# Kernel optimization log

Measured on AMD Instinct MI355X. Metric: run time of the kernel, lower is better.

The kernel has to match this reference:

```python
import jax, jax.numpy as jnp
import numpy as np

B, S, M, D, H, F, E, K = 4, 1024, 1024, 1024, 16, 4096, 4, 2
DH = D // H
LB_COEF = 0.01
LN_EPS = 1e-5


def setup_inputs() -> dict:
    key = jax.random.key(0)
    ks = jax.random.split(key, 16)
    w = lambda k, shape: jax.random.normal(k, shape, jnp.float32) * 0.02
    return {
        "x": jax.random.normal(ks[0], (B, S, D), jnp.float32),
        "memory": jax.random.normal(ks[1], (B, M, D), jnp.float32),
        "sWq": w(ks[2], (D, D)), "sWk": w(ks[3], (D, D)),
        "sWv": w(ks[4], (D, D)), "sWo": w(ks[5], (D, D)),
        "cWq": w(ks[6], (D, D)), "cWk": w(ks[7], (D, D)),
        "cWv": w(ks[8], (D, D)), "cWo": w(ks[9], (D, D)),
        "Wg": w(ks[10], (E, D)),
        "W1": w(ks[11], (E, F, D)), "b1": jnp.zeros((E, F), jnp.float32),
        "W2": w(ks[12], (E, D, F)), "b2": jnp.zeros((E, D), jnp.float32),
        "ln1_g": jnp.ones((D,), jnp.float32), "ln1_b": jnp.zeros((D,), jnp.float32),
        "ln2_g": jnp.ones((D,), jnp.float32), "ln2_b": jnp.zeros((D,), jnp.float32),
        "ln3_g": jnp.ones((D,), jnp.float32), "ln3_b": jnp.zeros((D,), jnp.float32),
    }


def _ln(x, g, b):
    m = x.mean(-1, keepdims=True)
    v = ((x - m) ** 2).mean(-1, keepdims=True)
    return (x - m) * jax.lax.rsqrt(v + LN_EPS) * g + b


def _mha(q_in, k_in, v_in, Wq, Wk, Wv, Wo):
    # nn.Linear(bias=False): y = x @ W.T; split into heads [b, h, s, dh]
    def split(t):
        b, s, _ = t.shape
        return t.reshape(b, s, H, DH).transpose(0, 2, 1, 3)
    Q = split(q_in @ Wq.T)
    Kh = split(k_in @ Wk.T)
    V = split(v_in @ Wv.T)
    scores = jnp.einsum('bhqd,bhkd->bhqk', Q, Kh) / jnp.sqrt(jnp.float32(DH))
    attn = jax.nn.softmax(scores, axis=-1)  # dropout is identity in eval
    out = jnp.einsum('bhqk,bhkd->bhqd', attn, V)
    b, _, s, _ = out.shape
    out = out.transpose(0, 2, 1, 3).reshape(b, s, D)
    return out @ Wo.T


def _moe(h, Wg, W1, b1, W2, b2):
    gate_logits = h @ Wg.T                      # [B, S, E]
    gate_probs = jax.nn.softmax(gate_logits, -1)
    topk_logits, topk_idx = jax.lax.top_k(gate_logits, K)
    topk_w = jax.nn.softmax(topk_logits, -1)    # [B, S, K]
    # dense all-experts FFN (faithful to source): [B, S, E, F] hidden
    hid = jax.nn.gelu(jnp.einsum('bsd,efd->bsef', h, W1) + b1, approximate=False)
    eo = jnp.einsum('bsef,edf->bsed', hid, W2) + b2   # [B, S, E, D]
    sel = jnp.take_along_axis(eo, topk_idx[..., None], axis=2)  # [B, S, K, D]
    out = (sel * topk_w[..., None]).sum(axis=2)
    one_hot = jax.nn.one_hot(topk_idx, E, dtype=gate_probs.dtype)  # [B, S, K, E]
    load = one_hot.sum(axis=2).mean(axis=(0, 1))   # [E]
    imp = gate_probs.mean(axis=(0, 1))             # [E]
    aux = LB_COEF * (E * jnp.sum(load * imp))
    return out, aux


def reference(x, memory, sWq, sWk, sWv, sWo, cWq, cWk, cWv, cWo,
              Wg, W1, b1, W2, b2,
              ln1_g, ln1_b, ln2_g, ln2_b, ln3_g, ln3_b):
    h = _ln(x, ln1_g, ln1_b)
    x = x + _mha(h, h, h, sWq, sWk, sWv, sWo)
    h = _ln(x, ln2_g, ln2_b)
    x = x + _mha(h, memory, memory, cWq, cWk, cWv, cWo)
    h = _ln(x, ln3_g, ln3_b)
    ffn_out, aux = _moe(h, Wg, W1, b1, W2, b2)
    return (x + ffn_out, aux)
```

## Files before the change

kernel.cpp:

```cpp
#include <hip/hip_runtime.h>
#include <math.h>
#include <stdint.h>

typedef unsigned short u16;
typedef _Float16 f16;
typedef __attribute__((ext_vector_type(8))) _Float16 f16x8;
typedef __attribute__((ext_vector_type(8))) short s16x8;
typedef __attribute__((ext_vector_type(4))) float f32x4;
typedef __attribute__((ext_vector_type(4))) unsigned short u16x4;

#define DEV static __device__ __forceinline__

#define MFMA16(a, b, c) __builtin_amdgcn_mfma_f32_16x16x32_f16((a), (b), (c), 0, 0, 0)

DEV void split2(float v, u16& hi, u16& lo) {
  f16 h = (f16)v;
  f16 l = (f16)(v - (float)h);
  hi = __builtin_bit_cast(u16, h);
  lo = __builtin_bit_cast(u16, l);
}
DEV u16 f2h(float v) { f16 h = (f16)v; return __builtin_bit_cast(u16, h); }
DEV float h2f(u16 u) { f16 h = __builtin_bit_cast(f16, u); return (float)h; }

DEV void gload16(const void* gp, const void* lp) {
  typedef const __attribute__((address_space(1))) unsigned GU;
  typedef __attribute__((address_space(3))) unsigned LU;
  GU* g = (GU*)(uintptr_t)gp;
  LU* l = (LU*)(unsigned)(uintptr_t)lp;
  __builtin_amdgcn_global_load_lds(g, l, 16, 0, 0);
}

DEV int swzP(int q) { return ((q & 3) << 4) ^ (((q >> 2) & 3) << 5); }


enum { EPI3_SPLIT = 0, EPI3_RESID = 1 };

template <int EPI>
__global__ __launch_bounds__(512, 4)
void gemm3(const u16* __restrict__ Ah, const u16* __restrict__ Al,
           const u16* __restrict__ Bh, const u16* __restrict__ Bl,
           int N, int K, int ldC,
           u16* __restrict__ outh, u16* __restrict__ outl,
           float* __restrict__ outf, const float* __restrict__ resid)
{
  __shared__ alignas(16) u16 sAh[2][128 * 32], sAl[2][128 * 32];
  __shared__ alignas(16) u16 sBh[2][128 * 32], sBl[2][128 * 32];
  const int tid = threadIdx.x;
  const int wave = tid >> 6, lane = tid & 63;
  const int wr = wave >> 2, wc = wave & 3;
  const int li = lane & 15, g = lane >> 4;
  const long row0 = (long)blockIdx.y * 128;
  const int col0 = blockIdx.x * 128;

  const int srow = tid >> 2;
  const int scol = ((tid & 3) ^ ((tid >> 3) & 3)) * 8;
  const long arow = (row0 + srow) * (long)K + scol;
  const long brow = ((long)col0 + srow) * (long)K + scol;
  const u16 *gAh = Ah + arow, *gAl = Al + arow;
  const u16 *gBh = Bh + brow, *gBl = Bl + brow;
  const int wbase = wave * 512;

  const f32x4 fz = {0.f, 0.f, 0.f, 0.f};
  f32x4 acc[4][2];
#pragma unroll
  for (int m = 0; m < 4; m++)
#pragma unroll
    for (int n = 0; n < 2; n++) acc[m][n] = fz;

  const int aoff = (wr * 64 + li) * 32 + (g ^ ((li >> 1) & 3)) * 8;
  const int boff = (wc * 32 + li) * 32 + (g ^ ((li >> 1) & 3)) * 8;

  gload16(gAh, &sAh[0][wbase]);
  gload16(gAl, &sAl[0][wbase]);
  gload16(gBh, &sBh[0][wbase]);
  gload16(gBl, &sBl[0][wbase]);

  int cur = 0;
  for (int k0 = 0; k0 < K; k0 += 32, cur ^= 1) {
    __syncthreads();
    const int nxt = cur ^ 1;
    if (k0 + 32 < K) {
      gload16(gAh + k0 + 32, &sAh[nxt][wbase]);
      gload16(gAl + k0 + 32, &sAl[nxt][wbase]);
      gload16(gBh + k0 + 32, &sBh[nxt][wbase]);
      gload16(gBl + k0 + 32, &sBl[nxt][wbase]);
    }
    f16x8 ah[4], al4[4], bh[2], bl4[2];
#pragma unroll
    for (int m = 0; m < 4; m++) {
      ah[m] = *(const f16x8*)(&sAh[cur][aoff + m * 512]);
      al4[m] = *(const f16x8*)(&sAl[cur][aoff + m * 512]);
    }
#pragma unroll
    for (int n = 0; n < 2; n++) {
      bh[n] = *(const f16x8*)(&sBh[cur][boff + n * 512]);
      bl4[n] = *(const f16x8*)(&sBl[cur][boff + n * 512]);
    }
#pragma unroll
    for (int m = 0; m < 4; m++)
#pragma unroll
      for (int n = 0; n < 2; n++) {
        f32x4 t = acc[m][n];
        t = MFMA16(al4[m], bh[n], t);
        t = MFMA16(ah[m], bl4[n], t);
        t = MFMA16(ah[m], bh[n], t);
        acc[m][n] = t;
      }
  }

#pragma unroll
  for (int m = 0; m < 4; m++)
#pragma unroll
    for (int n = 0; n < 2; n++) {
      const int col = col0 + wc * 32 + n * 16 + li;
#pragma unroll
      for (int r = 0; r < 4; r++) {
        const long row = row0 + wr * 64 + m * 16 + g * 4 + r;
        const long idx = row * ldC + col;
        const float v = acc[m][n][r];
        if constexpr (EPI == EPI3_SPLIT) {
          u16 hi, lo; split2(v, hi, lo);
          outh[idx] = hi; outl[idx] = lo;
        } else {
          outf[idx] = resid[idx] + v;
        }
      }
    }
}

__global__ __launch_bounds__(256)
void vtrans(const u16* __restrict__ Vh, const u16* __restrict__ Vl,
            u16* __restrict__ Th, u16* __restrict__ Tl)
{
  __shared__ u16 t0[64][80];
  __shared__ u16 t1[64][80];
  const int kb = blockIdx.x, h = blockIdx.y, b = blockIdx.z;
  const int tid = threadIdx.x;
  const int r = tid >> 2;
  const int c = tid & 3;
  const long srow = ((long)b * 1024 + kb * 64 + r) * 3072 + h * 64;
  s16x8 a0 = *(const s16x8*)(Vh + srow + c * 8);
  s16x8 a1 = *(const s16x8*)(Vh + srow + c * 8 + 32);
  s16x8 b0 = *(const s16x8*)(Vl + srow + c * 8);
  s16x8 b1 = *(const s16x8*)(Vl + srow + c * 8 + 32);
#pragma unroll
  for (int j = 0; j < 8; j++) {
    t0[c * 8 + j][r]      = (u16)(short)a0[j];
    t0[c * 8 + 32 + j][r] = (u16)(short)a1[j];
    t1[c * 8 + j][r]      = (u16)(short)b0[j];
    t1[c * 8 + 32 + j][r] = (u16)(short)b1[j];
  }
  __syncthreads();
  const int dh = tid >> 2;
  const long drow = ((long)(b * 16 + h) * 64 + dh) * 1024 + kb * 64;
  s16x8 o0, o1;
#pragma unroll
  for (int j = 0; j < 8; j++) {
    o0[j] = (short)t0[dh][c * 8 + j];
    o1[j] = (short)t0[dh][c * 8 + 32 + j];
  }
  *(s16x8*)(Th + drow + c * 8) = o0;
  *(s16x8*)(Th + drow + c * 8 + 32) = o1;
#pragma unroll
  for (int j = 0; j < 8; j++) {
    o0[j] = (short)t1[dh][c * 8 + j];
    o1[j] = (short)t1[dh][c * 8 + 32 + j];
  }
  *(s16x8*)(Tl + drow + c * 8) = o0;
  *(s16x8*)(Tl + drow + c * 8 + 32) = o1;
}

__global__ __launch_bounds__(512, 4)
void attn3(const u16* __restrict__ Qh, const u16* __restrict__ Ql,
           const u16* __restrict__ Kbh, const u16* __restrict__ Kbl,
           const u16* __restrict__ Vth, const u16* __restrict__ Vtl,
           u16* __restrict__ AOh, u16* __restrict__ AOl)
{
  __shared__ alignas(16) u16 lKh[64 * 64], lKl[64 * 64];
  __shared__ alignas(16) u16 lVh[64 * 64], lVl[64 * 64];
  __shared__ alignas(16) u16 lPh[8 * 16 * 64], lPl[8 * 16 * 64];
  const int tid = threadIdx.x;
  const int wave = tid >> 6, lane = tid & 63;
  const int li = lane & 15, g = lane >> 4;
  const int qt = blockIdx.x, h = blockIdx.y, b = blockIdx.z;
  const int bh = b * 16 + h;
  const int LD = 3072;

  const long qrow0 = (long)b * 1024 + qt * 128 + wave * 16;
  f16x8 qfh[2], qfl[2];
#pragma unroll
  for (int kk = 0; kk < 2; kk++) {
    const long qoff = (qrow0 + li) * LD + h * 64 + kk * 32 + g * 8;
    qfh[kk] = *(const f16x8*)(Qh + qoff);
    qfl[kk] = *(const f16x8*)(Ql + qoff);
  }

  const f32x4 fz = {0.f, 0.f, 0.f, 0.f};
  float m_run[4], l_run[4];
  f32x4 oacc[4];
#pragma unroll
  for (int r = 0; r < 4; r++) { m_run[r] = -INFINITY; l_run[r] = 0.f; }
#pragma unroll
  for (int d = 0; d < 4; d++) oacc[d] = fz;

  char* cKh = (char*)lKh; char* cKl = (char*)lKl;
  char* cVh = (char*)lVh; char* cVl = (char*)lVl;
  char* cPh = (char*)lPh + wave * 2048;
  char* cPl = (char*)lPl + wave * 2048;

  const int kr = tid >> 3;
  const int kce = (tid & 7) * 8;
  const u16* kbase_h = Kbh + ((long)b * 1024 + kr) * LD + h * 64 + kce;
  const u16* kbase_l = Kbl + ((long)b * 1024 + kr) * LD + h * 64 + kce;
  const u16* vbase_h = Vth + ((long)bh * 64 + kr) * 1024 + kce;
  const u16* vbase_l = Vtl + ((long)bh * 64 + kr) * 1024 + kce;
  const int sdst = kr * 128 + ((kce * 2) ^ ((kr & 7) << 4));

  s16x8 rkh, rkl, rvh, rvl;
#define LOADT(t)                                                   \
  {                                                                \
    const long ko = (long)(t) * 64 * LD;                           \
    const int vo = (t) * 64;                                       \
    rkh = *(const s16x8*)(kbase_h + ko);                           \
    rkl = *(const s16x8*)(kbase_l + ko);                           \
    rvh = *(const s16x8*)(vbase_h + vo);                           \
    rvl = *(const s16x8*)(vbase_l + vo);                           \
  }

  LOADT(0);

  for (int t = 0; t < 16; ++t) {
    __syncthreads();
    *(s16x8*)(cKh + sdst) = rkh;
    *(s16x8*)(cKl + sdst) = rkl;
    *(s16x8*)(cVh + sdst) = rvh;
    *(s16x8*)(cVl + sdst) = rvl;
    if (t < 15) LOADT(t + 1);
    __syncthreads();

    f32x4 s[4];
#pragma unroll
    for (int cb = 0; cb < 4; cb++) {
      f32x4 tt = fz;
      const int key = cb * 16 + li;
#pragma unroll
      for (int kk = 0; kk < 2; kk++) {
        const int off = key * 128 + (((kk * 32 + g * 8) * 2) ^ ((key & 7) << 4));
        f16x8 fh = *(const f16x8*)(cKh + off);
        f16x8 fl = *(const f16x8*)(cKl + off);
        tt = MFMA16(qfl[kk], fh, tt);
        tt = MFMA16(qfh[kk], fl, tt);
        tt = MFMA16(qfh[kk], fh, tt);
      }
      s[cb] = tt;
    }
#pragma unroll
    for (int cb = 0; cb < 4; cb++)
#pragma unroll
      for (int r = 0; r < 4; r++) s[cb][r] *= 0.125f;

#pragma unroll
    for (int r = 0; r < 4; r++) {
      float mx = fmaxf(fmaxf(s[0][r], s[1][r]), fmaxf(s[2][r], s[3][r]));
      mx = fmaxf(mx, __shfl_xor(mx, 1));
      mx = fmaxf(mx, __shfl_xor(mx, 2));
      mx = fmaxf(mx, __shfl_xor(mx, 4));
      mx = fmaxf(mx, __shfl_xor(mx, 8));
      float mnew = fmaxf(m_run[r], mx);
      float sc = __expf(m_run[r] - mnew);
      m_run[r] = mnew;
      float ls = 0.f;
#pragma unroll
      for (int cb = 0; cb < 4; cb++) {
        float p = __expf(s[cb][r] - mnew);
        s[cb][r] = p;
        ls += p;
      }
      ls += __shfl_xor(ls, 1);
      ls += __shfl_xor(ls, 2);
      ls += __shfl_xor(ls, 4);
      ls += __shfl_xor(ls, 8);
      l_run[r] = l_run[r] * sc + ls;
#pragma unroll
      for (int d = 0; d < 4; d++) oacc[d][r] *= sc;
    }

#pragma unroll
    for (int cb = 0; cb < 4; cb++)
#pragma unroll
      for (int r = 0; r < 4; r++) {
        const int q = g * 4 + r;
        const int key = cb * 16 + li;
        const int off = q * 128 + ((key * 2) ^ swzP(q));
        u16 hi, lo; split2(s[cb][r], hi, lo);
        *(u16*)(cPh + off) = hi;
        *(u16*)(cPl + off) = lo;
      }

#pragma unroll
    for (int kk = 0; kk < 2; kk++) {
      const int kbyte = (kk * 32 + g * 8) * 2;
      const int poff = li * 128 + (kbyte ^ swzP(li));
      f16x8 pfh = *(const f16x8*)(cPh + poff);
      f16x8 pfl = *(const f16x8*)(cPl + poff);
#pragma unroll
      for (int d = 0; d < 4; d++) {
        const int dh = d * 16 + li;
        const int voff = dh * 128 + (kbyte ^ ((dh & 7) << 4));
        f16x8 vfh = *(const f16x8*)(cVh + voff);
        f16x8 vfl = *(const f16x8*)(cVl + voff);
        f32x4 tacc = oacc[d];
        tacc = MFMA16(pfl, vfh, tacc);
        tacc = MFMA16(pfh, vfl, tacc);
        tacc = MFMA16(pfh, vfh, tacc);
        oacc[d] = tacc;
      }
    }
  }
#undef LOADT

#pragma unroll
  for (int d = 0; d < 4; d++)
#pragma unroll
    for (int r = 0; r < 4; r++) {
      const long row = qrow0 + g * 4 + r;
      const int col = h * 64 + d * 16 + li;
      u16 hi, lo; split2(oacc[d][r] / l_run[r], hi, lo);
      AOh[row * 1024 + col] = hi;
      AOl[row * 1024 + col] = lo;
    }
}

template <bool GATE>
__global__ __launch_bounds__(256)
void ln_kernel(const float* __restrict__ x, const float* __restrict__ gam,
               const float* __restrict__ bet, u16* __restrict__ hh,
               u16* __restrict__ hl,
               const float* __restrict__ Wg, float* __restrict__ glog)
{
  const int row = blockIdx.x;
  const int tid = threadIdx.x;
  const int wave = tid >> 6, lane = tid & 63;
  const float* xr = x + (long)row * 1024;
  float4 v = *(const float4*)(xr + tid * 4);
  float s = v.x + v.y + v.z + v.w;
  float s2 = v.x * v.x + v.y * v.y + v.z * v.z + v.w * v.w;
#pragma unroll
  for (int m = 1; m < 64; m <<= 1) { s += __shfl_xor(s, m); s2 += __shfl_xor(s2, m); }
  __shared__ float red1[4], red2[4];
  if (lane == 0) { red1[wave] = s; red2[wave] = s2; }
  __syncthreads();
  float S = red1[0] + red1[1] + red1[2] + red1[3];
  float S2 = red2[0] + red2[1] + red2[2] + red2[3];
  float mean = S * (1.f / 1024.f);
  float var = S2 * (1.f / 1024.f) - mean * mean;
  float rstd = 1.f / sqrtf(var + 1e-5f);
  const int c = tid * 4;
  float hv[4];
  hv[0] = (v.x - mean) * rstd * gam[c + 0] + bet[c + 0];
  hv[1] = (v.y - mean) * rstd * gam[c + 1] + bet[c + 1];
  hv[2] = (v.z - mean) * rstd * gam[c + 2] + bet[c + 2];
  hv[3] = (v.w - mean) * rstd * gam[c + 3] + bet[c + 3];
  u16x4 oh, ol;
#pragma unroll
  for (int j = 0; j < 4; j++) {
    u16 hi, lo; split2(hv[j], hi, lo);
    oh[j] = hi; ol[j] = lo;
  }
  *(u16x4*)(hh + (long)row * 1024 + c) = oh;
  *(u16x4*)(hl + (long)row * 1024 + c) = ol;

  if constexpr (GATE) {
    float pe[4];
#pragma unroll
    for (int e = 0; e < 4; e++) {
      const float* wr_ = Wg + e * 1024 + c;
      pe[e] = hv[0] * wr_[0] + hv[1] * wr_[1] + hv[2] * wr_[2] + hv[3] * wr_[3];
    }
#pragma unroll
    for (int e = 0; e < 4; e++)
#pragma unroll
      for (int m = 1; m < 64; m <<= 1) pe[e] += __shfl_xor(pe[e], m);
    __shared__ float gred[4][4];
    if (lane == 0) {
#pragma unroll
      for (int e = 0; e < 4; e++) gred[wave][e] = pe[e];
    }
    __syncthreads();
    if (tid < 4)
      glog[(long)row * 4 + tid] = gred[0][tid] + gred[1][tid] + gred[2][tid] + gred[3][tid];
  }
}

__global__ __launch_bounds__(256)
void route_kernel(const float* __restrict__ glog,
                  int* __restrict__ tlist, float* __restrict__ wrow,
                  int4* __restrict__ meta, float2* __restrict__ wts,
                  int* __restrict__ scanMeta, float* __restrict__ outAux)
{
  const int tid = threadIdx.x;
  const int lane = tid & 63, wave = tid >> 6;
  __shared__ int scn[4][256];
  __shared__ int sTot[4];
  __shared__ int sBase[4];
  __shared__ float sred[4][8];

  for (int r = tid; r < 8704; r += 256) { tlist[r] = 0; wrow[r] = 0.f; }

  int myCnt[4] = {0, 0, 0, 0};
  float imp[4] = {0.f, 0.f, 0.f, 0.f}, ld[4] = {0.f, 0.f, 0.f, 0.f};
  unsigned char e1s[16], e2s[16];
  float w1s[16], w2s[16];
#pragma unroll 1
  for (int j = 0; j < 16; j++) {
    const int t = tid * 16 + j;
    float l[4];
#pragma unroll
    for (int e = 0; e < 4; e++) l[e] = glog[t * 4 + e];
    int e1 = 0; float bv = l[0];
#pragma unroll
    for (int e = 1; e < 4; e++) if (l[e] > bv) { bv = l[e]; e1 = e; }
    int e2 = -1; float bv2 = -INFINITY;
#pragma unroll
    for (int e = 0; e < 4; e++) if (e != e1 && l[e] > bv2) { bv2 = l[e]; e2 = e; }
    float wq = expf(bv2 - bv);
    float w1 = 1.f / (1.f + wq), w2 = wq / (1.f + wq);
    float ps = 0.f, pv[4];
#pragma unroll
    for (int e = 0; e < 4; e++) { pv[e] = expf(l[e] - bv); ps += pv[e]; }
    float inv = 1.f / ps;
#pragma unroll
    for (int e = 0; e < 4; e++) imp[e] += pv[e] * inv;
    ld[e1] += 1.f; ld[e2] += 1.f;
    myCnt[e1]++; myCnt[e2]++;
    e1s[j] = (unsigned char)e1; e2s[j] = (unsigned char)e2;
    w1s[j] = w1; w2s[j] = w2;
  }
#pragma unroll
  for (int e = 0; e < 4; e++) scn[e][tid] = myCnt[e];
  __syncthreads();

  if (wave < 4) {
    int carry = 0;
    for (int seg = 0; seg < 4; seg++) {
      int v = scn[wave][seg * 64 + lane];
      const int orig = v;
#pragma unroll
      for (int d = 1; d < 64; d <<= 1) { int o = __shfl_up(v, d); if (lane >= d) v += o; }
      scn[wave][seg * 64 + lane] = carry + v - orig;
      carry += __shfl(v, 63);
    }
    if (lane == 0) sTot[wave] = carry;
  }
  __syncthreads();

  if (tid == 0) {
    int base = 0;
    for (int e = 0; e < 4; e++) {
      const int c = sTot[e];
      const int cap = (c + 127) & ~127;
      sBase[e] = base;
      const int t0 = base >> 7, t1 = (base + cap) >> 7;
      for (int i = t0; i < t1; i++) scanMeta[1 + i] = e;
      base += cap;
    }
    scanMeta[0] = base >> 7;
  }
  __syncthreads();

  int off[4];
#pragma unroll
  for (int e = 0; e < 4; e++) off[e] = sBase[e] + scn[e][tid];
#pragma unroll 1
  for (int j = 0; j < 16; j++) {
    const int t = tid * 16 + j;
    const int e1 = e1s[j], e2 = e2s[j];
    const int p1 = off[e1]++;
    const int p2 = off[e2]++;
    tlist[p1] = t; wrow[p1] = w1s[j];
    tlist[p2] = t; wrow[p2] = w2s[j];
    int4 m; m.x = p1; m.y = p2; m.z = e1; m.w = e2;
    meta[t] = m;
    float2 w; w.x = w1s[j]; w.y = w2s[j];
    wts[t] = w;
  }

#pragma unroll
  for (int e = 0; e < 4; e++) {
#pragma unroll
    for (int d = 1; d < 64; d <<= 1) {
      imp[e] += __shfl_xor(imp[e], d);
      ld[e] += __shfl_xor(ld[e], d);
    }
  }
  if (lane == 0) {
#pragma unroll
    for (int e = 0; e < 4; e++) { sred[wave][e] = imp[e]; sred[wave][4 + e] = ld[e]; }
  }
  __syncthreads();
  if (tid == 0) {
    float a = 0.f;
    for (int e = 0; e < 4; e++) {
      float im = sred[0][e] + sred[1][e] + sred[2][e] + sred[3][e];
      float lo = sred[0][4 + e] + sred[1][4 + e] + sred[2][4 + e] + sred[3][4 + e];
      a += (lo * (1.f / 4096.f)) * (im * (1.f / 4096.f));
    }
    outAux[0] = 0.01f * 4.f * a;
  }
}

__global__ __launch_bounds__(256, 2)
void gemm_up(const u16* __restrict__ A, const u16* __restrict__ w1h,
             const float* __restrict__ b1, const int* __restrict__ tlist,
             const float* __restrict__ wrow, const int* __restrict__ scanMeta,
             u16* __restrict__ hid)
{
  const int L = blockIdx.x;
  const int gg = (L & 7) * 272 + (L >> 3);
  const int rt = gg >> 5, cc = gg & 31;
  if (rt >= scanMeta[0]) return;
  const int e = scanMeta[1 + rt];
  __shared__ alignas(16) u16 lA[2][128 * 32];
  __shared__ alignas(16) u16 lB[2][128 * 32];
  const int tid = threadIdx.x;
  const int wave = tid >> 6, lane = tid & 63;
  const int wr = wave >> 1, wc = wave & 1;
  const int li = lane & 15, g = lane >> 4;
  const int row0 = rt * 128;
  const int col0 = cc * 128;

  const int srow = lane >> 2;
  const int scol = ((lane & 3) ^ ((lane >> 3) & 3)) * 8;
  const int r1 = row0 + wave * 32 + srow;
  const long t1 = tlist[r1], t2 = tlist[r1 + 16];
  const u16* gA1 = A + t1 * 1024 + scol;
  const u16* gA2 = A + t2 * 1024 + scol;
  const u16* gB = w1h + (size_t)e * 4194304 +
                  ((size_t)(col0 + wave * 32 + srow)) * 1024 + scol;
  const int wbase = wave * 1024;

  const f32x4 fz = {0.f, 0.f, 0.f, 0.f};
  f32x4 acc[4][4];
#pragma unroll
  for (int m = 0; m < 4; m++)
#pragma unroll
    for (int n = 0; n < 4; n++) acc[m][n] = fz;

  const int aoff = (wr * 64 + li) * 32 + (g ^ ((li >> 1) & 3)) * 8;
  const int boff = (wc * 64 + li) * 32 + (g ^ ((li >> 1) & 3)) * 8;

  gload16(gA1, &lA[0][wbase]);
  gload16(gA2, &lA[0][wbase + 512]);
  gload16(gB, &lB[0][wbase]);
  gload16(gB + 16 * 1024, &lB[0][wbase + 512]);

  int cur = 0;
  for (int k0 = 0; k0 < 1024; k0 += 32, cur ^= 1) {
    __syncthreads();
    const int nxt = cur ^ 1;
    if (k0 + 32 < 1024) {
      gload16(gA1 + k0 + 32, &lA[nxt][wbase]);
      gload16(gA2 + k0 + 32, &lA[nxt][wbase + 512]);
      gload16(gB + k0 + 32, &lB[nxt][wbase]);
      gload16(gB + k0 + 32 + 16 * 1024, &lB[nxt][wbase + 512]);
    }
    f16x8 af[4], bfr[4];
#pragma unroll
    for (int m = 0; m < 4; m++) af[m] = *(const f16x8*)(&lA[cur][aoff + m * 512]);
#pragma unroll
    for (int n = 0; n < 4; n++) bfr[n] = *(const f16x8*)(&lB[cur][boff + n * 512]);
#pragma unroll
    for (int m = 0; m < 4; m++)
#pragma unroll
      for (int n = 0; n < 4; n++)
        acc[m][n] = MFMA16(af[m], bfr[n], acc[m][n]);
  }

#pragma unroll
  for (int m = 0; m < 4; m++)
#pragma unroll
    for (int n = 0; n < 4; n++) {
      const int col = col0 + wc * 64 + n * 16 + li;
#pragma unroll
      for (int r = 0; r < 4; r++) {
        const int row = row0 + wr * 64 + m * 16 + g * 4 + r;
        const float coef = wrow[row];
        float tv = acc[m][n][r] + b1[e * 4096 + col];
        float ge = 0.5f * tv * (1.f + erff(tv * 0.7071067811865475f));
        hid[(size_t)row * 4096 + col] = f2h(coef * ge);
      }
    }
}

__global__ __launch_bounds__(512, 4)
void gemm_down(const u16* __restrict__ hid, const u16* __restrict__ w2h,
               const int* __restrict__ scanMeta, u16* __restrict__ part)
{
  const int L = blockIdx.x;
  const int gg = (L & 7) * 68 + (L >> 3);
  const int rt = gg >> 3, cc = gg & 7;
  if (rt >= scanMeta[0]) return;
  const int e = scanMeta[1 + rt];
  __shared__ alignas(16) u16 lA[2][128 * 32];
  __shared__ alignas(16) u16 lB[2][128 * 32];
  const int tid = threadIdx.x;
  const int wave = tid >> 6, lane = tid & 63;
  const int wr = wave >> 2, wc = wave & 3;
  const int li = lane & 15, g = lane >> 4;
  const int row0 = rt * 128;
  const int col0 = cc * 128;

  const int srow = tid >> 2;
  const int scol = ((tid & 3) ^ ((tid >> 3) & 3)) * 8;
  const u16* gA = hid + ((size_t)(row0 + srow)) * 4096 + scol;
  const u16* gB = w2h + (size_t)e * 4194304 +
                  ((size_t)(col0 + srow)) * 4096 + scol;
  const int wbase = wave * 512;

  const f32x4 fz = {0.f, 0.f, 0.f, 0.f};
  f32x4 acc[4][2];
#pragma unroll
  for (int m = 0; m < 4; m++)
#pragma unroll
    for (int n = 0; n < 2; n++) acc[m][n] = fz;

  const int aoff = (wr * 64 + li) * 32 + (g ^ ((li >> 1) & 3)) * 8;
  const int boff = (wc * 32 + li) * 32 + (g ^ ((li >> 1) & 3)) * 8;

  gload16(gA, &lA[0][wbase]);
  gload16(gB, &lB[0][wbase]);

  int cur = 0;
  for (int k0 = 0; k0 < 4096; k0 += 32, cur ^= 1) {
    __syncthreads();
    const int nxt = cur ^ 1;
    if (k0 + 32 < 4096) {
      gload16(gA + k0 + 32, &lA[nxt][wbase]);
      gload16(gB + k0 + 32, &lB[nxt][wbase]);
    }
    f16x8 af[4], bfr[2];
#pragma unroll
    for (int m = 0; m < 4; m++) af[m] = *(const f16x8*)(&lA[cur][aoff + m * 512]);
#pragma unroll
    for (int n = 0; n < 2; n++) bfr[n] = *(const f16x8*)(&lB[cur][boff + n * 512]);
#pragma unroll
    for (int m = 0; m < 4; m++)
#pragma unroll
      for (int n = 0; n < 2; n++)
        acc[m][n] = MFMA16(af[m], bfr[n], acc[m][n]);
  }

#pragma unroll
  for (int m = 0; m < 4; m++)
#pragma unroll
    for (int n = 0; n < 2; n++) {
      const int col = col0 + wc * 32 + n * 16 + li;
#pragma unroll
      for (int r = 0; r < 4; r++) {
        const int row = row0 + wr * 64 + m * 16 + g * 4 + r;
        part[(size_t)row * 1024 + col] = f2h(acc[m][n][r]);
      }
    }
}

__global__ __launch_bounds__(256)
void merge_kernel(const float* __restrict__ xw, const u16* __restrict__ part,
                  const int4* __restrict__ meta, const float2* __restrict__ wts,
                  const float* __restrict__ b2, float* __restrict__ out)
{
  const long i = ((long)blockIdx.x * 256 + threadIdx.x) * 4;
  const int row = (int)(i >> 10), col = (int)(i & 1023);
  const int4 m = meta[row];
  const float2 w = wts[row];
  float4 a = *(const float4*)(xw + i);
  u16x4 p1 = *(const u16x4*)(part + (size_t)m.x * 1024 + col);
  u16x4 p2 = *(const u16x4*)(part + (size_t)m.y * 1024 + col);
  const float* b2a = b2 + m.z * 1024 + col;
  const float* b2b = b2 + m.w * 1024 + col;
  float av[4] = {a.x, a.y, a.z, a.w};
  float4 o;
  float ov[4];
#pragma unroll
  for (int j = 0; j < 4; j++)
    ov[j] = av[j] + h2f(p1[j]) + h2f(p2[j]) + w.x * b2a[j] + w.y * b2b[j];
  o.x = ov[0]; o.y = ov[1]; o.z = ov[2]; o.w = ov[3];
  *(float4*)(out + i) = o;
}

__global__ __launch_bounds__(256)
void cvt_h(const float* __restrict__ src, u16* __restrict__ dst)
{
  const long i = ((long)blockIdx.x * 256 + threadIdx.x) * 4;
  float4 v = *(const float4*)(src + i);
  u16x4 o = {f2h(v.x), f2h(v.y), f2h(v.z), f2h(v.w)};
  *(u16x4*)(dst + i) = o;
}

__global__ __launch_bounds__(256)
void cvt_split(const float* __restrict__ src, u16* __restrict__ dh, u16* __restrict__ dl)
{
  const long i = ((long)blockIdx.x * 256 + threadIdx.x) * 4;
  float4 v = *(const float4*)(src + i);
  u16x4 oh, ol;
  float vv[4] = {v.x, v.y, v.z, v.w};
#pragma unroll
  for (int j = 0; j < 4; j++) { u16 a, b; split2(vv[j], a, b); oh[j] = a; ol[j] = b; }
  *(u16x4*)(dh + i) = oh;
  *(u16x4*)(dl + i) = ol;
}

struct Ptr8 { const float* p[8]; };

__global__ __launch_bounds__(256)
void cvt8_split(Ptr8 ps, u16* __restrict__ dh, u16* __restrict__ dl)
{
  const int w = blockIdx.y;
  const long i = ((long)blockIdx.x * 256 + threadIdx.x) * 4;
  float4 v = *(const float4*)(ps.p[w] + i);
  u16x4 oh, ol;
  float vv[4] = {v.x, v.y, v.z, v.w};
#pragma unroll
  for (int j = 0; j < 4; j++) { u16 a, b; split2(vv[j], a, b); oh[j] = a; ol[j] = b; }
  *(u16x4*)(dh + (long)w * 1048576 + i) = oh;
  *(u16x4*)(dl + (long)w * 1048576 + i) = ol;
}

extern "C" void kernel_launch(void* const* d_in, const int* in_sizes, int n_in,
                              void* d_out, int out_size, void* d_ws, size_t ws_size,
                              hipStream_t stream)
{
  const float* x    = (const float*)d_in[0];
  const float* mem  = (const float*)d_in[1];
  const float* sWq  = (const float*)d_in[2];
  const float* sWk  = (const float*)d_in[3];
  const float* sWv  = (const float*)d_in[4];
  const float* sWo  = (const float*)d_in[5];
  const float* cWq  = (const float*)d_in[6];
  const float* cWk  = (const float*)d_in[7];
  const float* cWv  = (const float*)d_in[8];
  const float* cWo  = (const float*)d_in[9];
  const float* Wg   = (const float*)d_in[10];
  const float* W1   = (const float*)d_in[11];
  const float* b1   = (const float*)d_in[12];
  const float* W2   = (const float*)d_in[13];
  const float* b2   = (const float*)d_in[14];
  const float* ln1g = (const float*)d_in[15];
  const float* ln1b = (const float*)d_in[16];
  const float* ln2g = (const float*)d_in[17];
  const float* ln2b = (const float*)d_in[18];
  const float* ln3g = (const float*)d_in[19];
  const float* ln3b = (const float*)d_in[20];
  float* out = (float*)d_out;
  (void)in_sizes; (void)n_in; (void)out_size; (void)ws_size;

  char* ws = (char*)d_ws;
  size_t off = 0;
  auto alloc = [&](size_t bytes) -> void* {
    void* p = ws + off; off += (bytes + 255) & ~(size_t)255; return p;
  };
  float* xw    = (float*)alloc((size_t)4096 * 1024 * 4);
  u16*   hh    = (u16*)  alloc((size_t)4096 * 1024 * 2);
  u16*   hl    = (u16*)  alloc((size_t)4096 * 1024 * 2);
  u16*   memh  = (u16*)  alloc((size_t)4096 * 1024 * 2);
  u16*   meml  = (u16*)  alloc((size_t)4096 * 1024 * 2);
  u16*   qkvh  = (u16*)  alloc((size_t)4096 * 3072 * 2);
  u16*   qkvl  = (u16*)  alloc((size_t)4096 * 3072 * 2);
  u16*   aoh   = (u16*)  alloc((size_t)4096 * 1024 * 2);
  u16*   aol   = (u16*)  alloc((size_t)4096 * 1024 * 2);
  u16*   aWh   = (u16*)  alloc((size_t)8 * 1024 * 1024 * 2);
  u16*   aWl   = (u16*)  alloc((size_t)8 * 1024 * 1024 * 2);
  u16*   w1h   = (u16*)  alloc((size_t)4 * 4096 * 1024 * 2);
  u16*   w2h   = (u16*)  alloc((size_t)4 * 4096 * 1024 * 2);
  float* glog  = (float*)alloc((size_t)4096 * 4 * 4);
  int*   tlist = (int*)  alloc((size_t)8704 * 4);
  float* wrow  = (float*)alloc((size_t)8704 * 4);
  int4*  meta  = (int4*) alloc((size_t)4096 * 16);
  float2* wts  = (float2*)alloc((size_t)4096 * 8);
  int*   scanM = (int*)  alloc((size_t)128 * 4);
  u16*   vth = hh;
  u16*   vtl = hl;
  u16*   hid = qkvh;
  u16*   part = (u16*)hh;

  Ptr8 p8;
  p8.p[0] = sWq; p8.p[1] = sWk; p8.p[2] = sWv; p8.p[3] = sWo;
  p8.p[4] = cWq; p8.p[5] = cWk; p8.p[6] = cWv; p8.p[7] = cWo;
  cvt8_split<<<dim3(1024, 8), 256, 0, stream>>>(p8, aWh, aWl);
  cvt_h<<<16384, 256, 0, stream>>>(W1, w1h);
  cvt_h<<<16384, 256, 0, stream>>>(W2, w2h);
  cvt_split<<<4096, 256, 0, stream>>>(mem, memh, meml);

  ln_kernel<false><<<4096, 256, 0, stream>>>(x, ln1g, ln1b, hh, hl, nullptr, nullptr);
  gemm3<EPI3_SPLIT><<<dim3(24, 32), 512, 0, stream>>>(hh, hl, aWh, aWl, 3072, 1024, 3072,
                                                      qkvh, qkvl, nullptr, nullptr);
  vtrans<<<dim3(16, 16, 4), 256, 0, stream>>>(qkvh + 2048, qkvl + 2048, vth, vtl);
  attn3<<<dim3(8, 16, 4), 512, 0, stream>>>(qkvh, qkvl, qkvh + 1024, qkvl + 1024,
                                            vth, vtl, aoh, aol);
  gemm3<EPI3_RESID><<<dim3(8, 32), 512, 0, stream>>>(aoh, aol, aWh + (size_t)3 * 1048576,
                                                     aWl + (size_t)3 * 1048576, 1024, 1024, 1024,
                                                     nullptr, nullptr, xw, x);

  ln_kernel<false><<<4096, 256, 0, stream>>>(xw, ln2g, ln2b, hh, hl, nullptr, nullptr);
  gemm3<EPI3_SPLIT><<<dim3(8, 32), 512, 0, stream>>>(hh, hl, aWh + (size_t)4 * 1048576,
                                                     aWl + (size_t)4 * 1048576, 1024, 1024, 3072,
                                                     qkvh, qkvl, nullptr, nullptr);
  gemm3<EPI3_SPLIT><<<dim3(16, 32), 512, 0, stream>>>(memh, meml, aWh + (size_t)5 * 1048576,
                                                      aWl + (size_t)5 * 1048576, 2048, 1024, 3072,
                                                      qkvh + 1024, qkvl + 1024, nullptr, nullptr);
  vtrans<<<dim3(16, 16, 4), 256, 0, stream>>>(qkvh + 2048, qkvl + 2048, vth, vtl);
  attn3<<<dim3(8, 16, 4), 512, 0, stream>>>(qkvh, qkvl, qkvh + 1024, qkvl + 1024,
                                            vth, vtl, aoh, aol);
  gemm3<EPI3_RESID><<<dim3(8, 32), 512, 0, stream>>>(aoh, aol, aWh + (size_t)7 * 1048576,
                                                     aWl + (size_t)7 * 1048576, 1024, 1024, 1024,
                                                     nullptr, nullptr, xw, xw);

  ln_kernel<true><<<4096, 256, 0, stream>>>(xw, ln3g, ln3b, hh, hl, Wg, glog);
  route_kernel<<<1, 256, 0, stream>>>(glog, tlist, wrow, meta, wts, scanM,
                                      out + (size_t)4096 * 1024);
  gemm_up<<<2176, 256, 0, stream>>>(hh, w1h, b1, tlist, wrow, scanM, hid);
  gemm_down<<<544, 512, 0, stream>>>(hid, w2h, scanM, part);
  merge_kernel<<<4096, 256, 0, stream>>>(xw, part, meta, wts, b2, out);
}
```

Measured before the change: 783.4 us.

## Triple-buffer LDS in MoE up/down GEMMs with explicit vmcnt waits

Both expert FFN GEMMs move from double to triple LDS buffers, keeping two tiles of global loads in flight. Each iteration now uses an explicit s_waitcnt vmcnt plus a raw s_barrier instead of __syncthreads, so the wait covers only the oldest tile. The goal is to hide global-load latency behind MFMA work. The cost is 1.5x LDS per block. Launch-bound occupancy hints are raised, which may pressure registers or fail to fit the LDS budget.

```diff
diff --git a/kernel.cpp b/kernel.cpp
--- a/kernel.cpp
+++ b/kernel.cpp
@@ -509,7 +509,7 @@
   }
 }
 
-__global__ __launch_bounds__(256, 2)
+__global__ __launch_bounds__(256, 3)
 void gemm_up(const u16* __restrict__ A, const u16* __restrict__ w1h,
              const float* __restrict__ b1, const int* __restrict__ tlist,
              const float* __restrict__ wrow, const int* __restrict__ scanMeta,
@@ -520,8 +520,8 @@
   const int rt = gg >> 5, cc = gg & 31;
   if (rt >= scanMeta[0]) return;
   const int e = scanMeta[1 + rt];
-  __shared__ alignas(16) u16 lA[2][128 * 32];
-  __shared__ alignas(16) u16 lB[2][128 * 32];
+  __shared__ alignas(16) u16 lA[3][128 * 32];
+  __shared__ alignas(16) u16 lB[3][128 * 32];
   const int tid = threadIdx.x;
   const int wave = tid >> 6, lane = tid & 63;
   const int wr = wave >> 1, wc = wave & 1;
@@ -549,20 +549,27 @@
   const int aoff = (wr * 64 + li) * 32 + (g ^ ((li >> 1) & 3)) * 8;
   const int boff = (wc * 64 + li) * 32 + (g ^ ((li >> 1) & 3)) * 8;
 
-  gload16(gA1, &lA[0][wbase]);
-  gload16(gA2, &lA[0][wbase + 512]);
-  gload16(gB, &lB[0][wbase]);
-  gload16(gB + 16 * 1024, &lB[0][wbase + 512]);
-
-  int cur = 0;
-  for (int k0 = 0; k0 < 1024; k0 += 32, cur ^= 1) {
-    __syncthreads();
-    const int nxt = cur ^ 1;
-    if (k0 + 32 < 1024) {
-      gload16(gA1 + k0 + 32, &lA[nxt][wbase]);
-      gload16(gA2 + k0 + 32, &lA[nxt][wbase + 512]);
-      gload16(gB + k0 + 32, &lB[nxt][wbase]);
-      gload16(gB + k0 + 32 + 16 * 1024, &lB[nxt][wbase + 512]);
+#define UP_ISSUE(i, bf)                                          \
+  {                                                              \
+    const int kk0 = (i) * 32;                                    \
+    gload16(gA1 + kk0, &lA[bf][wbase]);                          \
+    gload16(gA2 + kk0, &lA[bf][wbase + 512]);                    \
+    gload16(gB + kk0, &lB[bf][wbase]);                           \
+    gload16(gB + kk0 + 16 * 1024, &lB[bf][wbase + 512]);         \
+  }
+
+  UP_ISSUE(0, 0);
+  UP_ISSUE(1, 1);
+
+  for (int i = 0; i < 32; i++) {
+    if (i < 31) asm volatile("s_waitcnt vmcnt(4)" ::: "memory");
+    else        asm volatile("s_waitcnt vmcnt(0)" ::: "memory");
+    __builtin_amdgcn_s_barrier();
+    __builtin_amdgcn_sched_barrier(0);
+    const int cur = i % 3;
+    if (i + 2 < 32) {
+      const int nb = (i + 2) % 3;
+      UP_ISSUE(i + 2, nb);
     }
     f16x8 af[4], bfr[4];
 #pragma unroll
@@ -575,6 +582,7 @@
       for (int n = 0; n < 4; n++)
         acc[m][n] = MFMA16(af[m], bfr[n], acc[m][n]);
   }
+#undef UP_ISSUE
 
 #pragma unroll
   for (int m = 0; m < 4; m++)
@@ -592,7 +600,7 @@
     }
 }
 
-__global__ __launch_bounds__(512, 4)
+__global__ __launch_bounds__(512, 6)
 void gemm_down(const u16* __restrict__ hid, const u16* __restrict__ w2h,
                const int* __restrict__ scanMeta, u16* __restrict__ part)
 {
@@ -601,8 +609,8 @@
   const int rt = gg >> 3, cc = gg & 7;
   if (rt >= scanMeta[0]) return;
   const int e = scanMeta[1 + rt];
-  __shared__ alignas(16) u16 lA[2][128 * 32];
-  __shared__ alignas(16) u16 lB[2][128 * 32];
+  __shared__ alignas(16) u16 lA[3][128 * 32];
+  __shared__ alignas(16) u16 lB[3][128 * 32];
   const int tid = threadIdx.x;
   const int wave = tid >> 6, lane = tid & 63;
   const int wr = wave >> 2, wc = wave & 3;
@@ -627,16 +635,25 @@
   const int aoff = (wr * 64 + li) * 32 + (g ^ ((li >> 1) & 3)) * 8;
   const int boff = (wc * 32 + li) * 32 + (g ^ ((li >> 1) & 3)) * 8;
 
-  gload16(gA, &lA[0][wbase]);
-  gload16(gB, &lB[0][wbase]);
-
-  int cur = 0;
-  for (int k0 = 0; k0 < 4096; k0 += 32, cur ^= 1) {
-    __syncthreads();
-    const int nxt = cur ^ 1;
-    if (k0 + 32 < 4096) {
-      gload16(gA + k0 + 32, &lA[nxt][wbase]);
-      gload16(gB + k0 + 32, &lB[nxt][wbase]);
+#define DN_ISSUE(i, bf)                                          \
+  {                                                              \
+    const int kk0 = (i) * 32;                                    \
+    gload16(gA + kk0, &lA[bf][wbase]);                           \
+    gload16(gB + kk0, &lB[bf][wbase]);                           \
+  }
+
+  DN_ISSUE(0, 0);
+  DN_ISSUE(1, 1);
+
+  for (int i = 0; i < 128; i++) {
+    if (i < 127) asm volatile("s_waitcnt vmcnt(2)" ::: "memory");
+    else         asm volatile("s_waitcnt vmcnt(0)" ::: "memory");
+    __builtin_amdgcn_s_barrier();
+    __builtin_amdgcn_sched_barrier(0);
+    const int cur = i % 3;
+    if (i + 2 < 128) {
+      const int nb = (i + 2) % 3;
+      DN_ISSUE(i + 2, nb);
     }
     f16x8 af[4], bfr[2];
 #pragma unroll
@@ -649,6 +666,7 @@
       for (int n = 0; n < 2; n++)
         acc[m][n] = MFMA16(af[m], bfr[n], acc[m][n]);
   }
+#undef DN_ISSUE
 
 #pragma unroll
   for (int m = 0; m < 4; m++)
```

Result: no change. 798.5 us (+1.9%).
